# Kernel tuning notes

Measured on AMD Instinct MI355X. Metric: run time of the kernel, lower is better.

Reference implementation:

```python
import jax, jax.numpy as jnp
import numpy as np
from jax import lax

B, T = 64, 512
VOCAB, E = 16000, 128
USCRIPT, UE = 64, 16
F, MAX_NGRAM = 128, 5
C = 13  # num_classes


def setup_inputs() -> dict:
    key = jax.random.key(0)
    ks = jax.random.split(key, 18)
    inp = {
        "input_char": jax.random.randint(ks[0], (B, T), 0, VOCAB),
        "input_script": jax.random.randint(ks[1], (B, T), 0, USCRIPT),
        "input_mask": jnp.ones((B, T), dtype=bool),
        "char_emb": jax.random.normal(ks[2], (VOCAB, E), jnp.float32) * 0.02,
        "uscript_emb": jax.random.normal(ks[3], (USCRIPT, UE), jnp.float32) * 0.02,
        "dense_w": jax.random.normal(ks[4], (MAX_NGRAM * F + UE, C), jnp.float32) * 0.05,
        "dense_b": jnp.zeros((C,), jnp.float32),
        "trans": jax.random.normal(ks[5], (C, C), jnp.float32) * 0.1,
        "left_b": jax.random.normal(ks[6], (C,), jnp.float32) * 0.1,
        "right_b": jax.random.normal(ks[7], (C,), jnp.float32) * 0.1,
    }
    for i in range(1, MAX_NGRAM + 1):
        inp[f"conv_w{i}"] = jax.random.normal(ks[7 + i], (i, E, F), jnp.float32) * (1.0 / np.sqrt(i * E))
        inp[f"conv_b{i}"] = jnp.zeros((F,), jnp.float32)
    return inp


def _conv1d_same_relu(x, w, b):
    # x: [B,T,Cin], w: [K,Cin,Cout]
    y = lax.conv_general_dilated(x, w, window_strides=(1,), padding="SAME",
                                 dimension_numbers=("NWC", "WIO", "NWC"))
    return jax.nn.relu(y + b)


def _potentials(input_char, input_script, input_mask, char_emb, uscript_emb,
                conv_ws, conv_bs, dense_w, dense_b, left_b, right_b):
    emb = char_emb[input_char]              # [B,T,E]
    uemb = uscript_emb[input_script]        # [B,T,UE]
    feats = [_conv1d_same_relu(emb, w, b) for w, b in zip(conv_ws, conv_bs)]
    ctx = jnp.concatenate(feats + [uemb], axis=-1)          # [B,T,5F+UE]
    pot = jnp.einsum("btf,fc->btc", ctx, dense_w) + dense_b  # [B,T,C]
    # boundary energies (tfa CRF use_boundary=True): add left_b at first
    # valid step, right_b at last valid step per the mask
    m = input_mask.astype(pot.dtype)[..., None]              # [B,T,1]
    prev_m = jnp.pad(m[:, :-1], ((0, 0), (1, 0), (0, 0)))
    next_m = jnp.pad(m[:, 1:], ((0, 0), (0, 1), (0, 0)))
    pot = pot + m * (1.0 - prev_m) * left_b + m * (1.0 - next_m) * right_b
    return pot


def _viterbi_decode(pot, trans):
    # pot: [B,T,C], trans: [C,C]; full-length sequences (mask all ones)
    def fwd(state, pot_t):
        scores = state[:, :, None] + trans[None]   # [B, prev, cur]
        bp = jnp.argmax(scores, axis=1)            # [B,C]
        state = jnp.max(scores, axis=1) + pot_t    # [B,C]
        return state, bp

    final, bps = lax.scan(fwd, pot[:, 0], jnp.swapaxes(pot[:, 1:], 0, 1))
    last = jnp.argmax(final, axis=-1)              # [B]

    def back(tag, bp_t):
        prev = jnp.take_along_axis(bp_t, tag[:, None], axis=1)[:, 0]
        return prev, prev

    _, tags = lax.scan(back, last, bps, reverse=True)  # [T-1, B], forward order
    decoded = jnp.concatenate([jnp.swapaxes(tags, 0, 1), last[:, None]], axis=1)
    return decoded.astype(jnp.int32)


def reference(input_char, input_script, input_mask, char_emb, uscript_emb,
              conv_w1, conv_b1, conv_w2, conv_b2, conv_w3, conv_b3,
              conv_w4, conv_b4, conv_w5, conv_b5,
              dense_w, dense_b, trans, left_b, right_b):
    conv_ws = [conv_w1, conv_w2, conv_w3, conv_w4, conv_w5]
    conv_bs = [conv_b1, conv_b2, conv_b3, conv_b4, conv_b5]
    pot = _potentials(input_char, input_script, input_mask, char_emb, uscript_emb,
                      conv_ws, conv_bs, dense_w, dense_b, left_b, right_b)
    seq_len = jnp.sum(input_mask.astype(jnp.int32), axis=1)
    decoded = _viterbi_decode(pot, trans)
    return decoded, pot, seq_len, trans
```

## Files before the change

### kernel.cpp

```cpp
#include <hip/hip_runtime.h>

#define NB 64
#define NT 512
#define NC 13
#define AP 136
#define WP 72
#define PT 516
#define USTRIDE 18432
#define DWT_H   552960
#define DWT_L   563200
#define WS_NEED 1146880

typedef short s8v __attribute__((ext_vector_type(8)));
typedef float f4v __attribute__((ext_vector_type(4)));
typedef unsigned short ush;
typedef unsigned int u32;

__device__ __forceinline__ ush f2bf(float f){
    union { float f; u32 u; } v; v.f = f;
    u32 r = v.u + 0x7fffu + ((v.u >> 16) & 1u);
    return (ush)(r >> 16);
}
__device__ __forceinline__ float bf2f(ush h){
    union { u32 u; float f; } v; v.u = ((u32)h) << 16; return v.f;
}

__global__ __launch_bounds__(512)
void prep_kernel(const float* __restrict__ cw1, const float* __restrict__ cw2,
                 const float* __restrict__ cw3, const float* __restrict__ cw4,
                 const float* __restrict__ cw5, const float* __restrict__ dense_w,
                 ush* __restrict__ ws)
{
    int bx = blockIdx.x, tid = threadIdx.x;
    if (bx < 30) {
        int u = bx, ut = u >> 1, eh = u & 1;
        int fb = ut<1?0: ut<3?1: ut<6?2: ut<10?3:4;
        int jj = ut - fb*(fb+1)/2;
        const float* cw = fb==0?cw1: fb==1?cw2: fb==2?cw3: fb==3?cw4: cw5;
        #pragma unroll
        for (int it = 0; it < 2; ++it) {
            int g = it*512 + tid;
            int f = g & 127;
            int e8 = (g >> 7) << 3;
            float v[8];
            #pragma unroll
            for (int q = 0; q < 8; ++q)
                v[q] = cw[(jj*128 + eh*64 + e8 + q)*128 + f];
            ush h8[8], l8[8];
            #pragma unroll
            for (int q = 0; q < 8; ++q) {
                h8[q] = f2bf(v[q]);
                l8[q] = f2bf(v[q] - bf2f(h8[q]));
            }
            uint4 hv, lv;
            hv.x = h8[0] | ((u32)h8[1]<<16); hv.y = h8[2] | ((u32)h8[3]<<16);
            hv.z = h8[4] | ((u32)h8[5]<<16); hv.w = h8[6] | ((u32)h8[7]<<16);
            lv.x = l8[0] | ((u32)l8[1]<<16); lv.y = l8[2] | ((u32)l8[3]<<16);
            lv.z = l8[4] | ((u32)l8[5]<<16); lv.w = l8[6] | ((u32)l8[7]<<16);
            *(uint4*)&ws[u*USTRIDE + f*WP + e8]        = hv;
            *(uint4*)&ws[u*USTRIDE + 9216 + f*WP + e8] = lv;
        }
    } else {
        int fb = bx - 30;
        #pragma unroll
        for (int it = 0; it < 4; ++it) {
            int idx = it*512 + tid;
            int c = idx >> 7, f = idx & 127;
            float v = (c < 13) ? dense_w[(fb*128 + f)*13 + c] : 0.f;
            ush hi = f2bf(v);
            ws[DWT_H + fb*2048 + idx] = hi;
            ws[DWT_L + fb*2048 + idx] = f2bf(v - bf2f(hi));
        }
    }
}

__global__ __launch_bounds__(512)
void pot_kernel_ws(const int* __restrict__ input_char,
                   const int* __restrict__ input_script,
                   const float* __restrict__ char_emb,
                   const float* __restrict__ uscript_emb,
                   const float* __restrict__ dense_w,
                   const float* __restrict__ dense_b,
                   const float* __restrict__ left_b,
                   const float* __restrict__ right_b,
                   const float* __restrict__ cb1, const float* __restrict__ cb2,
                   const float* __restrict__ cb3, const float* __restrict__ cb4,
                   const float* __restrict__ cb5,
                   const ush* __restrict__ ws,
                   float* __restrict__ out_pot)
{
    __shared__ __align__(16) ush smem[77280];
    ush* Ah     = smem;
    ush* Al     = smem + 17952;
    ush* feat_h = smem + 54336;
    ush* feat_l = smem + 63040;
    float* uebt = (float*)(smem + 72768);
    float* dwue = (float*)(smem + 76864);

    const int tid  = threadIdx.x;
    const int lane = tid & 63;
    const int wid  = tid >> 6;
    const int tg   = wid >> 2;
    const int fg   = wid & 3;
    const int lr   = lane & 15;
    const int lq   = lane >> 4;
    const int bb   = blockIdx.x >> 2;
    const int t0   = (blockIdx.x & 3) << 7;

    {
        const char* g = (const char*)ws;
        char* l = (char*)(smem + 35904);
        #pragma unroll
        for (int i = 0; i < 5; ++i) {
            int idx = wid + (i << 3);
            if (i < 4 || wid < 4)
                __builtin_amdgcn_global_load_lds(
                    (const __attribute__((address_space(1))) void*)(g + idx*1024 + lane*16),
                    (__attribute__((address_space(3))) void*)(l + idx*1024 + lane*16), 16, 0, 0);
        }
    }

    for (int i = tid; i < 132*16; i += 512) {
        int row = i >> 4, s = (i & 15) << 3;
        int t = t0 + row - 2;
        uint4 hv = {0,0,0,0}, lv = {0,0,0,0};
        if (t >= 0 && t < NT) {
            int ch = input_char[bb*NT + t];
            const float* src = char_emb + ch*128 + s;
            float4 x0 = *(const float4*)src;
            float4 x1 = *(const float4*)(src + 4);
            float fs[8] = {x0.x,x0.y,x0.z,x0.w,x1.x,x1.y,x1.z,x1.w};
            ush h[8], l[8];
            #pragma unroll
            for (int q = 0; q < 8; ++q) {
                h[q] = f2bf(fs[q]);
                l[q] = f2bf(fs[q] - bf2f(h[q]));
            }
            hv.x = h[0] | ((u32)h[1]<<16); hv.y = h[2] | ((u32)h[3]<<16);
            hv.z = h[4] | ((u32)h[5]<<16); hv.w = h[6] | ((u32)h[7]<<16);
            lv.x = l[0] | ((u32)l[1]<<16); lv.y = l[2] | ((u32)l[3]<<16);
            lv.z = l[4] | ((u32)l[5]<<16); lv.w = l[6] | ((u32)l[7]<<16);
        }
        *(uint4*)&Ah[row*AP + s] = hv;
        *(uint4*)&Al[row*AP + s] = lv;
    }
    for (int i = tid; i < 2048; i += 512) {
        int uu = i >> 7, tl = i & 127;
        uebt[uu*128 + tl] = uscript_emb[input_script[bb*NT + t0 + tl]*16 + uu];
    }
    if (tid < 208) dwue[tid] = dense_w[640*13 + tid];
    __syncthreads();

    const float* cbs[5] = {cb1, cb2, cb3, cb4, cb5};

    f4v cacc[4][2];
    #pragma unroll
    for (int mt = 0; mt < 4; ++mt)
        #pragma unroll
        for (int nt = 0; nt < 2; ++nt) cacc[mt][nt] = (f4v){0.f,0.f,0.f,0.f};
    f4v dacc = (f4v){0.f,0.f,0.f,0.f};

    #pragma unroll 1
    for (int u = 0; u < 30; ++u) {
        int ut  = u >> 1, eh = u & 1;
        int fb  = ut<1?0: ut<3?1: ut<6?2: ut<10?3:4;
        int jj  = ut - fb*(fb+1)/2;
        int jsh = (2 - (fb >> 1)) + jj;

        if (u < 29) {
            const char* g = (const char*)ws + (u + 1)*36864;
            char* l = (char*)(smem + (((u + 1) & 1) ? 54336 : 35904));
            #pragma unroll
            for (int i = 0; i < 5; ++i) {
                int idx = wid + (i << 3);
                if (i < 4 || wid < 4)
                    __builtin_amdgcn_global_load_lds(
                        (const __attribute__((address_space(1))) void*)(g + idx*1024 + lane*16),
                        (__attribute__((address_space(3))) void*)(l + idx*1024 + lane*16), 16, 0, 0);
            }
        }

        const ush* Wh = smem + ((u & 1) ? 54336 : 35904);
        const ush* Wl = Wh + 9216;
        #pragma unroll
        for (int kk = 0; kk < 2; ++kk) {
            int ko = kk*32 + (lq << 3);
            s8v bh[2], bl[2];
            #pragma unroll
            for (int nt = 0; nt < 2; ++nt) {
                int frow = fg*32 + nt*16 + lr;
                bh[nt] = *(const s8v*)&Wh[frow*WP + ko];
                bl[nt] = *(const s8v*)&Wl[frow*WP + ko];
            }
            #pragma unroll
            for (int mt = 0; mt < 4; ++mt) {
                int row = tg*64 + mt*16 + lr + jsh;
                int ai  = row*AP + eh*64 + ko;
                s8v ah = *(const s8v*)&Ah[ai];
                s8v al = *(const s8v*)&Al[ai];
                #pragma unroll
                for (int nt = 0; nt < 2; ++nt) {
                    cacc[mt][nt] = __builtin_amdgcn_mfma_f32_16x16x32_bf16(ah, bh[nt], cacc[mt][nt], 0,0,0);
                    cacc[mt][nt] = __builtin_amdgcn_mfma_f32_16x16x32_bf16(ah, bl[nt], cacc[mt][nt], 0,0,0);
                    cacc[mt][nt] = __builtin_amdgcn_mfma_f32_16x16x32_bf16(al, bh[nt], cacc[mt][nt], 0,0,0);
                }
            }
        }

        if (u == 1 || u == 5 || u == 11 || u == 19 || u == 29) {
            __syncthreads();
            float cbv0 = cbs[fb][fg*32 + lr];
            float cbv1 = cbs[fb][fg*32 + 16 + lr];

            #pragma unroll 1
            for (int h = 0; h < 2; ++h) {
                if (tg == h) {
                    #pragma unroll
                    for (int mt = 0; mt < 4; ++mt)
                        #pragma unroll
                        for (int nt = 0; nt < 2; ++nt)
                            #pragma unroll
                            for (int r = 0; r < 4; ++r) {
                                float v = fmaxf(cacc[mt][nt][r] + (nt ? cbv1 : cbv0), 0.f);
                                int rw = mt*16 + (lq << 2) + r;
                                int f  = fg*32 + nt*16 + lr;
                                ush hh = f2bf(v);
                                feat_h[rw*AP + f] = hh;
                                feat_l[rw*AP + f] = f2bf(v - bf2f(hh));
                            }
                }
                __syncthreads();
                if (tg == h) {
                    int trow = fg*16 + lr;
                    #pragma unroll
                    for (int kf = 0; kf < 4; ++kf) {
                        int f0 = kf*32 + (lq << 3);
                        s8v a2h = *(const s8v*)&ws[DWT_H + fb*2048 + lr*128 + f0];
                        s8v a2l = *(const s8v*)&ws[DWT_L + fb*2048 + lr*128 + f0];
                        s8v b2h = *(const s8v*)&feat_h[trow*AP + f0];
                        s8v b2l = *(const s8v*)&feat_l[trow*AP + f0];
                        dacc = __builtin_amdgcn_mfma_f32_16x16x32_bf16(a2h, b2h, dacc, 0,0,0);
                        dacc = __builtin_amdgcn_mfma_f32_16x16x32_bf16(a2h, b2l, dacc, 0,0,0);
                        dacc = __builtin_amdgcn_mfma_f32_16x16x32_bf16(a2l, b2h, dacc, 0,0,0);
                    }
                    if (fb == 4) {
                        int tloc  = tg*64 + fg*16 + lr;
                        int tglob = t0 + tloc;
                        float pc[4];
                        #pragma unroll
                        for (int r = 0; r < 4; ++r) pc[r] = dacc[r];
                        #pragma unroll
                        for (int uu = 0; uu < 16; ++uu) {
                            float uv = uebt[uu*128 + tloc];
                            #pragma unroll
                            for (int r = 0; r < 4; ++r) {
                                int c = (lq << 2) + r;
                                if (c < 13) pc[r] = fmaf(uv, dwue[uu*13 + c], pc[r]);
                            }
                        }
                        #pragma unroll
                        for (int r = 0; r < 4; ++r) {
                            int c = (lq << 2) + r;
                            if (c < 13) {
                                float v = pc[r] + dense_b[c];
                                if (tglob == 0)    v += left_b[c];
                                if (tglob == NT-1) v += right_b[c];
                                out_pot[(bb*NT + tglob)*13 + c] = v;
                            }
                        }
                    }
                }
                __syncthreads();
            }
            #pragma unroll
            for (int mt = 0; mt < 4; ++mt)
                #pragma unroll
                for (int nt = 0; nt < 2; ++nt) cacc[mt][nt] = (f4v){0.f,0.f,0.f,0.f};
        } else {
            __syncthreads();
        }
    }
}

__global__ __launch_bounds__(512)
void pot_kernel_fb(const int* __restrict__ input_char,
                   const int* __restrict__ input_script,
                   const float* __restrict__ char_emb,
                   const float* __restrict__ uscript_emb,
                   const float* __restrict__ dense_w,
                   const float* __restrict__ dense_b,
                   const float* __restrict__ left_b,
                   const float* __restrict__ right_b,
                   const float* __restrict__ cw1, const float* __restrict__ cb1,
                   const float* __restrict__ cw2, const float* __restrict__ cb2,
                   const float* __restrict__ cw3, const float* __restrict__ cb3,
                   const float* __restrict__ cw4, const float* __restrict__ cb4,
                   const float* __restrict__ cw5, const float* __restrict__ cb5,
                   float* __restrict__ out_pot)
{
    __shared__ __align__(16) ush smem[71744];
    ush* Ah     = smem;
    ush* Al     = smem + 17952;
    ush* Wh     = smem + 35904;
    ush* Wl     = smem + 45120;
    ush* feat_h = smem + 54336;
    ush* feat_l = smem + 63040;
    float* dwlds = (float*)(smem + 35904);
    float* dwue  = (float*)(smem + 39232);
    float* uebt  = (float*)(smem + 39648);

    const int tid  = threadIdx.x;
    const int lane = tid & 63;
    const int wid  = tid >> 6;
    const int tg   = wid >> 2;
    const int fg   = wid & 3;
    const int lr   = lane & 15;
    const int lq   = lane >> 4;
    const int bb   = blockIdx.x >> 2;
    const int t0   = (blockIdx.x & 3) << 7;

    for (int i = tid; i < 132*16; i += 512) {
        int row = i >> 4, s = (i & 15) << 3;
        int t = t0 + row - 2;
        uint4 hv = {0,0,0,0}, lv = {0,0,0,0};
        if (t >= 0 && t < NT) {
            int ch = input_char[bb*NT + t];
            const float* src = char_emb + ch*128 + s;
            float4 x0 = *(const float4*)src;
            float4 x1 = *(const float4*)(src + 4);
            float fs[8] = {x0.x,x0.y,x0.z,x0.w,x1.x,x1.y,x1.z,x1.w};
            ush h[8], l[8];
            #pragma unroll
            for (int q = 0; q < 8; ++q) {
                h[q] = f2bf(fs[q]);
                l[q] = f2bf(fs[q] - bf2f(h[q]));
            }
            hv.x = h[0] | ((u32)h[1]<<16); hv.y = h[2] | ((u32)h[3]<<16);
            hv.z = h[4] | ((u32)h[5]<<16); hv.w = h[6] | ((u32)h[7]<<16);
            lv.x = l[0] | ((u32)l[1]<<16); lv.y = l[2] | ((u32)l[3]<<16);
            lv.z = l[4] | ((u32)l[5]<<16); lv.w = l[6] | ((u32)l[7]<<16);
        }
        *(uint4*)&Ah[row*AP + s] = hv;
        *(uint4*)&Al[row*AP + s] = lv;
    }

    const float* cws[5] = {cw1, cw2, cw3, cw4, cw5};
    const float* cbs[5] = {cb1, cb2, cb3, cb4, cb5};

    f4v cacc[4][2];
    #pragma unroll
    for (int mt = 0; mt < 4; ++mt)
        #pragma unroll
        for (int nt = 0; nt < 2; ++nt) cacc[mt][nt] = (f4v){0.f,0.f,0.f,0.f};
    f4v dacc = (f4v){0.f,0.f,0.f,0.f};

    #pragma unroll 1
    for (int u = 0; u < 30; ++u) {
        int ut  = u >> 1, eh = u & 1;
        int fb  = ut<1?0: ut<3?1: ut<6?2: ut<10?3:4;
        int jj  = ut - fb*(fb+1)/2;
        int jsh = (2 - (fb >> 1)) + jj;
        const float* cw = cws[fb] + (jj*128 + eh*64)*128;

        __syncthreads();
        for (int g = tid; g < 1024; g += 512) {
            int f = g & 127, e8 = (g >> 7) << 3;
            float v[8];
            #pragma unroll
            for (int q = 0; q < 8; ++q) v[q] = cw[(e8 + q)*128 + f];
            ush h8[8], l8[8];
            #pragma unroll
            for (int q = 0; q < 8; ++q) {
                h8[q] = f2bf(v[q]);
                l8[q] = f2bf(v[q] - bf2f(h8[q]));
            }
            uint4 hv, lv;
            hv.x = h8[0] | ((u32)h8[1]<<16); hv.y = h8[2] | ((u32)h8[3]<<16);
            hv.z = h8[4] | ((u32)h8[5]<<16); hv.w = h8[6] | ((u32)h8[7]<<16);
            lv.x = l8[0] | ((u32)l8[1]<<16); lv.y = l8[2] | ((u32)l8[3]<<16);
            lv.z = l8[4] | ((u32)l8[5]<<16); lv.w = l8[6] | ((u32)l8[7]<<16);
            *(uint4*)&Wh[f*WP + e8] = hv;
            *(uint4*)&Wl[f*WP + e8] = lv;
        }
        __syncthreads();

        #pragma unroll
        for (int kk = 0; kk < 2; ++kk) {
            int ko = kk*32 + (lq << 3);
            s8v bh[2], bl[2];
            #pragma unroll
            for (int nt = 0; nt < 2; ++nt) {
                int frow = fg*32 + nt*16 + lr;
                bh[nt] = *(const s8v*)&Wh[frow*WP + ko];
                bl[nt] = *(const s8v*)&Wl[frow*WP + ko];
            }
            #pragma unroll
            for (int mt = 0; mt < 4; ++mt) {
                int row = tg*64 + mt*16 + lr + jsh;
                int ai  = row*AP + eh*64 + ko;
                s8v ah = *(const s8v*)&Ah[ai];
                s8v al = *(const s8v*)&Al[ai];
                #pragma unroll
                for (int nt = 0; nt < 2; ++nt) {
                    cacc[mt][nt] = __builtin_amdgcn_mfma_f32_16x16x32_bf16(ah, bh[nt], cacc[mt][nt], 0,0,0);
                    cacc[mt][nt] = __builtin_amdgcn_mfma_f32_16x16x32_bf16(ah, bl[nt], cacc[mt][nt], 0,0,0);
                    cacc[mt][nt] = __builtin_amdgcn_mfma_f32_16x16x32_bf16(al, bh[nt], cacc[mt][nt], 0,0,0);
                }
            }
        }

        if (u == 1 || u == 5 || u == 11 || u == 19 || u == 29) {
            __syncthreads();
            for (int i = tid; i < 128*13; i += 512)
                dwlds[i] = dense_w[fb*128*13 + i];
            if (fb == 4) {
                for (int i = tid; i < 16*13; i += 512)
                    dwue[i] = dense_w[640*13 + i];
                for (int i = tid; i < 2048; i += 512) {
                    int uu = i >> 7, tl = i & 127;
                    uebt[uu*128 + tl] = uscript_emb[input_script[bb*NT + t0 + tl]*16 + uu];
                }
            }
            __syncthreads();

            float cbv0 = cbs[fb][fg*32 + lr];
            float cbv1 = cbs[fb][fg*32 + 16 + lr];

            #pragma unroll 1
            for (int h = 0; h < 2; ++h) {
                if (tg == h) {
                    #pragma unroll
                    for (int mt = 0; mt < 4; ++mt)
                        #pragma unroll
                        for (int nt = 0; nt < 2; ++nt)
                            #pragma unroll
                            for (int r = 0; r < 4; ++r) {
                                float v = fmaxf(cacc[mt][nt][r] + (nt ? cbv1 : cbv0), 0.f);
                                int rw = mt*16 + (lq << 2) + r;
                                int f  = fg*32 + nt*16 + lr;
                                ush hh = f2bf(v);
                                feat_h[rw*AP + f] = hh;
                                feat_l[rw*AP + f] = f2bf(v - bf2f(hh));
                            }
                }
                __syncthreads();
                if (tg == h) {
                    int trow = fg*16 + lr;
                    #pragma unroll
                    for (int kf = 0; kf < 4; ++kf) {
                        int f0 = kf*32 + (lq << 3);
                        float dv[8];
                        #pragma unroll
                        for (int q = 0; q < 8; ++q) dv[q] = dwlds[(f0 + q)*13 + lr];
                        s8v a2h, a2l;
                        #pragma unroll
                        for (int q = 0; q < 8; ++q) {
                            ush hh = f2bf(dv[q]);
                            a2h[q] = (short)hh;
                            a2l[q] = (short)f2bf(dv[q] - bf2f(hh));
                        }
                        s8v b2h = *(const s8v*)&feat_h[trow*AP + f0];
                        s8v b2l = *(const s8v*)&feat_l[trow*AP + f0];
                        dacc = __builtin_amdgcn_mfma_f32_16x16x32_bf16(a2h, b2h, dacc, 0,0,0);
                        dacc = __builtin_amdgcn_mfma_f32_16x16x32_bf16(a2h, b2l, dacc, 0,0,0);
                        dacc = __builtin_amdgcn_mfma_f32_16x16x32_bf16(a2l, b2h, dacc, 0,0,0);
                    }
                    if (fb == 4) {
                        int tloc  = tg*64 + fg*16 + lr;
                        int tglob = t0 + tloc;
                        float pc[4];
                        #pragma unroll
                        for (int r = 0; r < 4; ++r) pc[r] = dacc[r];
                        #pragma unroll
                        for (int uu = 0; uu < 16; ++uu) {
                            float uv = uebt[uu*128 + tloc];
                            #pragma unroll
                            for (int r = 0; r < 4; ++r) {
                                int c = (lq << 2) + r;
                                if (c < 13) pc[r] = fmaf(uv, dwue[uu*13 + c], pc[r]);
                            }
                        }
                        #pragma unroll
                        for (int r = 0; r < 4; ++r) {
                            int c = (lq << 2) + r;
                            if (c < 13) {
                                float v = pc[r] + dense_b[c];
                                if (tglob == 0)    v += left_b[c];
                                if (tglob == NT-1) v += right_b[c];
                                out_pot[(bb*NT + tglob)*13 + c] = v;
                            }
                        }
                    }
                }
                __syncthreads();
            }
            #pragma unroll
            for (int mt = 0; mt < 4; ++mt)
                #pragma unroll
                for (int nt = 0; nt < 2; ++nt) cacc[mt][nt] = (f4v){0.f,0.f,0.f,0.f};
        }
    }
}

#define DPPF(dst, src, ctrl) \
    dst = __int_as_float(__builtin_amdgcn_mov_dpp(__float_as_int(src), ctrl, 0xF, 0xF, false))

__global__ __launch_bounds__(256)
void viterbi_kernel(const float* __restrict__ pot,
                    const float* __restrict__ trans,
                    float* __restrict__ out_dec,
                    float* __restrict__ out_seq,
                    float* __restrict__ out_trans)
{
    __shared__ __align__(16) float s_lds[NT * NC];
    __shared__ __align__(16) float ptld[16 * PT];
    __shared__ float t_lds[NC * NC];
    __shared__ unsigned char path_lds[16 * 13 * 32];
    __shared__ unsigned char entry_lds[16 * 13];
    __shared__ int chunk_e[16];

    const int b   = blockIdx.x;
    const int tid = threadIdx.x;

    for (int i = tid; i < 3 * PT; i += 256) ptld[13 * PT + i] = 0.f;
    for (int i = tid; i < NT * NC; i += 256) {
        int t = i / NC, c = i - t * NC;
        float v = pot[b * NT * NC + i];
        ptld[c * PT + t] = v;
        if (t == 0) s_lds[c] = v;
    }
    for (int i = tid; i < NC * NC; i += 256) t_lds[i] = trans[i];
    __syncthreads();

    if (tid < 16) {
        const int c = tid;
        int r1 = __builtin_amdgcn_mov_dpp(c, 0x121, 0xF, 0xF, false);
        const bool fwd = (r1 == ((c + 1) & 15));
        float tc[16];
        #pragma unroll
        for (int k = 0; k < 16; ++k) {
            int p = fwd ? ((c + k) & 15) : ((c - k) & 15);
            tc[k] = (c < 13 && p < 13) ? t_lds[p * NC + c] : -1e30f;
        }
        float s = (c < 13) ? s_lds[c] : -1e30f;
        int t = 1;

        auto step = [&](float pv) {
            float v0 = s, v1, v2, v3, v4, v5, v6, v7;
            float v8, v9, v10, v11, v12, v13, v14, v15;
            DPPF(v1, v0, 0x121);
            DPPF(v2, v0, 0x122); DPPF(v3, v1, 0x122);
            DPPF(v4, v0, 0x124); DPPF(v5, v1, 0x124);
            DPPF(v6, v2, 0x124); DPPF(v7, v3, 0x124);
            DPPF(v8,  v0, 0x128); DPPF(v9,  v1, 0x128);
            DPPF(v10, v2, 0x128); DPPF(v11, v3, 0x128);
            DPPF(v12, v4, 0x128); DPPF(v13, v5, 0x128);
            DPPF(v14, v6, 0x128); DPPF(v15, v7, 0x128);
            float m0 = fmaxf(v0  + tc[0],  v1  + tc[1]);
            float m1 = fmaxf(v2  + tc[2],  v3  + tc[3]);
            float m2 = fmaxf(v4  + tc[4],  v5  + tc[5]);
            float m3 = fmaxf(v6  + tc[6],  v7  + tc[7]);
            float m4 = fmaxf(v8  + tc[8],  v9  + tc[9]);
            float m5 = fmaxf(v10 + tc[10], v11 + tc[11]);
            float m6 = fmaxf(v12 + tc[12], v13 + tc[13]);
            float m7 = fmaxf(v14 + tc[14], v15 + tc[15]);
            float n0 = fmaxf(m0, m1), n1 = fmaxf(m2, m3);
            float n2 = fmaxf(m4, m5), n3 = fmaxf(m6, m7);
            s = fmaxf(fmaxf(n0, n1), fmaxf(n2, n3)) + pv;
            if (c < 13) s_lds[t * NC + c] = s;
            ++t;
        };

        const float* prow = &ptld[c * PT];
        float4 pvv = *(const float4*)&prow[4];
        step(prow[1]);
        step(prow[2]);
        step(prow[3]);
        #pragma unroll 1
        for (int t4 = 4; t4 < NT; t4 += 4) {
            float4 cur = pvv;
            if (t4 + 4 < NT) pvv = *(const float4*)&prow[t4 + 4];
            step(cur.x); step(cur.y); step(cur.z); step(cur.w);
        }
    }
    __syncthreads();

    if (tid < 16 * 13) {
        const int chunk = tid / 13;
        const int e     = tid - chunk * 13;
        unsigned char* path = &path_lds[(chunk * 13 + e) * 32];
        int cur = e;
        path[31] = (unsigned char)e;
        for (int tl = 31; tl >= 1; --tl) {
            const float* srow = &s_lds[(chunk * 32 + tl - 1) * NC];
            float best = -1e30f; int bi = 0;
            #pragma unroll
            for (int p = 0; p < NC; ++p) {
                float v = srow[p] + t_lds[p * NC + cur];
                if (v > best) { best = v; bi = p; }
            }
            cur = bi;
            path[tl - 1] = (unsigned char)cur;
        }
        if (chunk > 0) {
            const float* srow = &s_lds[(chunk * 32 - 1) * NC];
            float best = -1e30f; int bi = 0;
            #pragma unroll
            for (int p = 0; p < NC; ++p) {
                float v = srow[p] + t_lds[p * NC + cur];
                if (v > best) { best = v; bi = p; }
            }
            entry_lds[chunk * 13 + e] = (unsigned char)bi;
        }
    }
    __syncthreads();

    if (tid == 0) {
        float best = -1e30f; int last = 0;
        for (int c = 0; c < NC; ++c) {
            float v = s_lds[(NT - 1) * NC + c];
            if (v > best) { best = v; last = c; }
        }
        chunk_e[15] = last;
        for (int i = 15; i >= 1; --i)
            chunk_e[i - 1] = entry_lds[i * 13 + chunk_e[i]];
    }
    __syncthreads();

    float* dec = out_dec + b * NT;
    for (int t = tid; t < NT; t += 256) {
        int ck = t >> 5;
        dec[t] = (float)path_lds[(ck * 13 + chunk_e[ck]) * 32 + (t & 31)];
    }
    if (tid == 0) out_seq[b] = (float)NT;
    if (b == 0) {
        for (int i = tid; i < NC * NC; i += 256) out_trans[i] = trans[i];
    }
}

extern "C" void kernel_launch(void* const* d_in, const int* in_sizes, int n_in,
                              void* d_out, int out_size, void* d_ws, size_t ws_size,
                              hipStream_t stream) {
    const int*   input_char   = (const int*)d_in[0];
    const int*   input_script = (const int*)d_in[1];
    const float* char_emb     = (const float*)d_in[3];
    const float* uscript_emb  = (const float*)d_in[4];
    const float* dense_w      = (const float*)d_in[5];
    const float* dense_b      = (const float*)d_in[6];
    const float* trans        = (const float*)d_in[7];
    const float* left_b       = (const float*)d_in[8];
    const float* right_b      = (const float*)d_in[9];
    const float* cw1 = (const float*)d_in[10];
    const float* cb1 = (const float*)d_in[11];
    const float* cw2 = (const float*)d_in[12];
    const float* cb2 = (const float*)d_in[13];
    const float* cw3 = (const float*)d_in[14];
    const float* cb3 = (const float*)d_in[15];
    const float* cw4 = (const float*)d_in[16];
    const float* cb4 = (const float*)d_in[17];
    const float* cw5 = (const float*)d_in[18];
    const float* cb5 = (const float*)d_in[19];

    float* out       = (float*)d_out;
    float* out_dec   = out;
    float* out_pot   = out + NB * NT;
    float* out_seq   = out_pot + NB * NT * NC;
    float* out_trans = out_seq + NB;

    if (ws_size >= (size_t)WS_NEED) {
        hipLaunchKernelGGL(prep_kernel, dim3(35), dim3(512), 0, stream,
                           cw1, cw2, cw3, cw4, cw5, dense_w, (ush*)d_ws);
        hipLaunchKernelGGL(pot_kernel_ws, dim3(256), dim3(512), 0, stream,
                           input_char, input_script, char_emb, uscript_emb,
                           dense_w, dense_b, left_b, right_b,
                           cb1, cb2, cb3, cb4, cb5,
                           (const ush*)d_ws, out_pot);
    } else {
        hipLaunchKernelGGL(pot_kernel_fb, dim3(256), dim3(512), 0, stream,
                           input_char, input_script, char_emb, uscript_emb,
                           dense_w, dense_b, left_b, right_b,
                           cw1, cb1, cw2, cb2, cw3, cb3, cw4, cb4, cw5, cb5,
                           out_pot);
    }

    hipLaunchKernelGGL(viterbi_kernel, dim3(NB), dim3(256), 0, stream,
                       out_pot, trans, out_dec, out_seq, out_trans);
}
```

Baseline: 155.7 us.

## Split Viterbi into forward scan kernel and separate chunked backtrack kernel

Splits the single Viterbi kernel into two. A scan kernel runs the 16-lane DPP forward recurrence and writes every score row to workspace memory, and a backtrack kernel reloads those rows and does the chunk-parallel backtracking. The goal is to free the forward scan from the LDS traffic, occupancy limits and block-wide synchronisation of the monolithic kernel. The cost is an extra launch plus a 2 MB round trip through global memory. The old fused kernel is kept as a fallback when the workspace is too small.

```diff
diff --git a/kernel.cpp b/kernel.cpp
--- a/kernel.cpp
+++ b/kernel.cpp
@@ -10,6 +10,8 @@
 #define DWT_H   552960
 #define DWT_L   563200
 #define WS_NEED 1146880
+#define WS_SROWS 1146880
+#define WS_NEED2 (WS_SROWS + NB*NT*16*4)
 
 typedef short s8v __attribute__((ext_vector_type(8)));
 typedef float f4v __attribute__((ext_vector_type(4)));
@@ -506,11 +508,161 @@
     dst = __int_as_float(__builtin_amdgcn_mov_dpp(__float_as_int(src), ctrl, 0xF, 0xF, false))
 
 __global__ __launch_bounds__(256)
-void viterbi_kernel(const float* __restrict__ pot,
-                    const float* __restrict__ trans,
-                    float* __restrict__ out_dec,
-                    float* __restrict__ out_seq,
-                    float* __restrict__ out_trans)
+void scan_kernel(const float* __restrict__ pot,
+                 const float* __restrict__ trans,
+                 float* __restrict__ srows)
+{
+    __shared__ __align__(16) float ptld[16 * PT];
+    __shared__ float t_lds[NC * NC];
+
+    const int b   = blockIdx.x;
+    const int tid = threadIdx.x;
+
+    for (int i = tid; i < 3 * PT; i += 256) ptld[13 * PT + i] = 0.f;
+    for (int i = tid; i < NT * NC; i += 256) {
+        int t = i / NC, c = i - t * NC;
+        ptld[c * PT + t] = pot[b * NT * NC + i];
+    }
+    for (int i = tid; i < NC * NC; i += 256) t_lds[i] = trans[i];
+    __syncthreads();
+
+    if (tid >= 16) return;
+    const int c = tid;
+    int r1 = __builtin_amdgcn_mov_dpp(c, 0x121, 0xF, 0xF, false);
+    const bool fwd = (r1 == ((c + 1) & 15));
+    float tc[16];
+    #pragma unroll
+    for (int k = 0; k < 16; ++k) {
+        int p = fwd ? ((c + k) & 15) : ((c - k) & 15);
+        tc[k] = (c < 13 && p < 13) ? t_lds[p * NC + c] : -1e30f;
+    }
+    float s = (c < 13) ? ptld[c * PT] : -1e30f;
+    float* srb = srows + b * NT * 16;
+    srb[c] = s;
+    int t = 1;
+
+    auto step = [&](float pv) {
+        float v0 = s, v1, v2, v3, v4, v5, v6, v7;
+        float v8, v9, v10, v11, v12, v13, v14, v15;
+        DPPF(v1, v0, 0x121);
+        DPPF(v2, v0, 0x122); DPPF(v3, v1, 0x122);
+        DPPF(v4, v0, 0x124); DPPF(v5, v1, 0x124);
+        DPPF(v6, v2, 0x124); DPPF(v7, v3, 0x124);
+        DPPF(v8,  v0, 0x128); DPPF(v9,  v1, 0x128);
+        DPPF(v10, v2, 0x128); DPPF(v11, v3, 0x128);
+        DPPF(v12, v4, 0x128); DPPF(v13, v5, 0x128);
+        DPPF(v14, v6, 0x128); DPPF(v15, v7, 0x128);
+        float m0 = fmaxf(v0  + tc[0],  v1  + tc[1]);
+        float m1 = fmaxf(v2  + tc[2],  v3  + tc[3]);
+        float m2 = fmaxf(v4  + tc[4],  v5  + tc[5]);
+        float m3 = fmaxf(v6  + tc[6],  v7  + tc[7]);
+        float m4 = fmaxf(v8  + tc[8],  v9  + tc[9]);
+        float m5 = fmaxf(v10 + tc[10], v11 + tc[11]);
+        float m6 = fmaxf(v12 + tc[12], v13 + tc[13]);
+        float m7 = fmaxf(v14 + tc[14], v15 + tc[15]);
+        float n0 = fmaxf(m0, m1), n1 = fmaxf(m2, m3);
+        float n2 = fmaxf(m4, m5), n3 = fmaxf(m6, m7);
+        s = fmaxf(fmaxf(n0, n1), fmaxf(n2, n3)) + pv;
+        srb[t * 16 + c] = s;
+        ++t;
+    };
+
+    const float* prow = &ptld[c * PT];
+    float4 pvv = *(const float4*)&prow[4];
+    step(prow[1]);
+    step(prow[2]);
+    step(prow[3]);
+    #pragma unroll 1
+    for (int t4 = 4; t4 < NT; t4 += 4) {
+        float4 cur = pvv;
+        if (t4 + 4 < NT) pvv = *(const float4*)&prow[t4 + 4];
+        step(cur.x); step(cur.y); step(cur.z); step(cur.w);
+    }
+}
+
+__global__ __launch_bounds__(256)
+void backtrack_kernel(const float* __restrict__ srows,
+                      const float* __restrict__ trans,
+                      float* __restrict__ out_dec,
+                      float* __restrict__ out_seq,
+                      float* __restrict__ out_trans)
+{
+    __shared__ __align__(16) float sl[NT * 16];
+    __shared__ float t_lds[NC * NC];
+    __shared__ unsigned char path_lds[16 * 13 * 32];
+    __shared__ unsigned char entry_lds[16 * 13];
+    __shared__ int chunk_e[16];
+
+    const int b   = blockIdx.x;
+    const int tid = threadIdx.x;
+
+    {
+        const float4* src = reinterpret_cast<const float4*>(srows + b * NT * 16);
+        float4* dst = reinterpret_cast<float4*>(sl);
+        for (int i = tid; i < NT * 16 / 4; i += 256) dst[i] = src[i];
+        for (int i = tid; i < NC * NC; i += 256) t_lds[i] = trans[i];
+    }
+    __syncthreads();
+
+    if (tid < 16 * 13) {
+        const int chunk = tid / 13;
+        const int e     = tid - chunk * 13;
+        unsigned char* path = &path_lds[(chunk * 13 + e) * 32];
+        int cur = e;
+        path[31] = (unsigned char)e;
+        for (int tl = 31; tl >= 1; --tl) {
+            const float* srow = &sl[(chunk * 32 + tl - 1) * 16];
+            float best = -1e30f; int bi = 0;
+            #pragma unroll
+            for (int p = 0; p < NC; ++p) {
+                float v = srow[p] + t_lds[p * NC + cur];
+                if (v > best) { best = v; bi = p; }
+            }
+            cur = bi;
+            path[tl - 1] = (unsigned char)cur;
+        }
+        if (chunk > 0) {
+            const float* srow = &sl[(chunk * 32 - 1) * 16];
+            float best = -1e30f; int bi = 0;
+            #pragma unroll
+            for (int p = 0; p < NC; ++p) {
+                float v = srow[p] + t_lds[p * NC + cur];
+                if (v > best) { best = v; bi = p; }
+            }
+            entry_lds[chunk * 13 + e] = (unsigned char)bi;
+        }
+    }
+    __syncthreads();
+
+    if (tid == 0) {
+        float best = -1e30f; int last = 0;
+        for (int c = 0; c < NC; ++c) {
+            float v = sl[(NT - 1) * 16 + c];
+            if (v > best) { best = v; last = c; }
+        }
+        chunk_e[15] = last;
+        for (int i = 15; i >= 1; --i)
+            chunk_e[i - 1] = entry_lds[i * 13 + chunk_e[i]];
+    }
+    __syncthreads();
+
+    float* dec = out_dec + b * NT;
+    for (int t = tid; t < NT; t += 256) {
+        int ck = t >> 5;
+        dec[t] = (float)path_lds[(ck * 13 + chunk_e[ck]) * 32 + (t & 31)];
+    }
+    if (tid == 0) out_seq[b] = (float)NT;
+    if (b == 0) {
+        for (int i = tid; i < NC * NC; i += 256) out_trans[i] = trans[i];
+    }
+}
+
+__global__ __launch_bounds__(256)
+void viterbi_mono(const float* __restrict__ pot,
+                  const float* __restrict__ trans,
+                  float* __restrict__ out_dec,
+                  float* __restrict__ out_seq,
+                  float* __restrict__ out_trans)
 {
     __shared__ __align__(16) float s_lds[NT * NC];
     __shared__ __align__(16) float ptld[16 * PT];
@@ -667,7 +819,10 @@
     float* out_seq   = out_pot + NB * NT * NC;
     float* out_trans = out_seq + NB;
 
-    if (ws_size >= (size_t)WS_NEED) {
+    bool have_prep = ws_size >= (size_t)WS_NEED;
+    bool have_srow = ws_size >= (size_t)WS_NEED2;
+
+    if (have_prep) {
         hipLaunchKernelGGL(prep_kernel, dim3(35), dim3(512), 0, stream,
                            cw1, cw2, cw3, cw4, cw5, dense_w, (ush*)d_ws);
         hipLaunchKernelGGL(pot_kernel_ws, dim3(256), dim3(512), 0, stream,
@@ -683,6 +838,14 @@
                            out_pot);
     }
 
-    hipLaunchKernelGGL(viterbi_kernel, dim3(NB), dim3(256), 0, stream,
-                       out_pot, trans, out_dec, out_seq, out_trans);
+    if (have_srow) {
+        float* srows = (float*)((char*)d_ws + WS_SROWS);
+        hipLaunchKernelGGL(scan_kernel, dim3(NB), dim3(256), 0, stream,
+                           out_pot, trans, srows);
+        hipLaunchKernelGGL(backtrack_kernel, dim3(NB), dim3(256), 0, stream,
+                           srows, trans, out_dec, out_seq, out_trans);
+    } else {
+        hipLaunchKernelGGL(viterbi_mono, dim3(NB), dim3(256), 0, stream,
+                           out_pot, trans, out_dec, out_seq, out_trans);
+    }
 }
```

New measurement: 158.2 us. About the same (+1.6%).
